# Kernel optimization log

Measured on AMD Instinct MI355X. Metric: run time of the kernel, lower is better.

The kernel has to match this reference:

```python
import jax, jax.numpy as jnp
import numpy as np

N = 10000      # nodes
E = 320000     # edges
IN_DIM = 256
HID = 256
EDGE_DIM = 64


def _sage(x, src, dst, w_l, b_l, w_r, n_nodes):
    """PyG SAGEConv (aggr='mean', root_weight=True, normalize=False):
    out_i = lin_l(mean_{j->i} x_j) + lin_r(x_i). Messages flow src->dst."""
    msg = x[src]                                            # [E, F]
    agg = jax.ops.segment_sum(msg, dst, num_segments=n_nodes)
    cnt = jax.ops.segment_sum(jnp.ones((msg.shape[0], 1), x.dtype), dst,
                              num_segments=n_nodes)
    mean = agg / jnp.maximum(cnt, 1.0)                      # [N, F]
    return mean @ w_l.T + b_l + x @ w_r.T                   # [N, HID]


def setup_inputs() -> dict:
    key = jax.random.key(0)
    ks = jax.random.split(key, 13)
    s = 0.02
    return {
        "x": jax.random.normal(ks[0], (N, IN_DIM), dtype=jnp.float32),
        "edge_attr": jax.random.normal(ks[1], (E, EDGE_DIM), dtype=jnp.float32),
        "conv1_wl": jax.random.normal(ks[2], (HID, IN_DIM), dtype=jnp.float32) * s,
        "conv1_bl": jnp.zeros((HID,), dtype=jnp.float32),
        "conv1_wr": jax.random.normal(ks[3], (HID, IN_DIM), dtype=jnp.float32) * s,
        "conv2_wl": jax.random.normal(ks[4], (HID, HID), dtype=jnp.float32) * s,
        "conv2_bl": jnp.zeros((HID,), dtype=jnp.float32),
        "conv2_wr": jax.random.normal(ks[5], (HID, HID), dtype=jnp.float32) * s,
        "mlp_w1": jax.random.normal(ks[6], (HID, 2 * HID + EDGE_DIM), dtype=jnp.float32) * s,
        "mlp_b1": jnp.zeros((HID,), dtype=jnp.float32),
        "mlp_w2": jax.random.normal(ks[7], (1, HID), dtype=jnp.float32) * s,
        "mlp_b2": jnp.zeros((1,), dtype=jnp.float32),
        "edge_index": jax.random.randint(ks[8], (2, E), 0, N, dtype=jnp.int32),
    }


def reference(x, edge_attr, conv1_wl, conv1_bl, conv1_wr,
              conv2_wl, conv2_bl, conv2_wr,
              mlp_w1, mlp_b1, mlp_w2, mlp_b2, edge_index):
    src, dst = edge_index[0], edge_index[1]
    # encode_nodes (dropout is identity in eval mode)
    h = jax.nn.relu(_sage(x, src, dst, conv1_wl, conv1_bl, conv1_wr, N))
    h = _sage(h, src, dst, conv2_wl, conv2_bl, conv2_wr, N)
    # edge_logits: gather endpoints, concat with edge_attr, 2-layer MLP
    feats = jnp.concatenate([h[src], h[dst], edge_attr], axis=1)   # [E, 2H+ED]
    hidden = jax.nn.relu(feats @ mlp_w1.T + mlp_b1)                # [E, H]
    logits = hidden @ mlp_w2.T + mlp_b2                            # [E, 1]
    return logits[:, 0]
```

## Files before the change

### kernel.cpp

```cpp
#include <hip/hip_runtime.h>

#define N_NODES 10000
#define N_EDGES 320000
#define DIM 256
#define ED 64
#define W1_LD 576

__global__ void hist_kernel(const int* __restrict__ dst, int* __restrict__ cnt, int n) {
  int i = blockIdx.x * blockDim.x + threadIdx.x;
  if (i < n) atomicAdd(&cnt[dst[i]], 1);
}

__global__ void scan_kernel(const int* __restrict__ cnt, int* __restrict__ off,
                            int* __restrict__ cursor, int n) {
  __shared__ int sm[256];
  __shared__ int carry_s;
  if (threadIdx.x == 0) carry_s = 0;
  __syncthreads();
  for (int base = 0; base < n; base += 256) {
    int i = base + threadIdx.x;
    int v = (i < n) ? cnt[i] : 0;
    sm[threadIdx.x] = v;
    __syncthreads();
    #pragma unroll
    for (int s = 1; s < 256; s <<= 1) {
      int t = (threadIdx.x >= s) ? sm[threadIdx.x - s] : 0;
      __syncthreads();
      sm[threadIdx.x] += t;
      __syncthreads();
    }
    int excl = sm[threadIdx.x] - v + carry_s;
    if (i < n) { off[i] = excl; cursor[i] = excl; }
    __syncthreads();
    if (threadIdx.x == 0) carry_s += sm[255];
    __syncthreads();
  }
  if (threadIdx.x == 0) off[n] = carry_s;
}

__global__ void scatter_kernel(const int* __restrict__ src, const int* __restrict__ dst,
                               int* __restrict__ cursor, int* __restrict__ csr_src, int n) {
  int i = blockIdx.x * blockDim.x + threadIdx.x;
  if (i < n) {
    int p = atomicAdd(&cursor[dst[i]], 1);
    csr_src[p] = src[i];
  }
}

__global__ __launch_bounds__(256) void aggregate_kernel(
    const float* __restrict__ X, const int* __restrict__ off,
    const int* __restrict__ csr_src, float* __restrict__ out) {
  int node = blockIdx.x * 4 + (threadIdx.x >> 6);
  if (node >= N_NODES) return;
  int t4 = (threadIdx.x & 63) * 4;
  int beg = off[node], end = off[node + 1];
  float ax = 0.f, ay = 0.f, az = 0.f, aw = 0.f;
  int e = beg;
  for (; e + 1 < end; e += 2) {
    int s0 = csr_src[e], s1 = csr_src[e + 1];
    float4 v0 = *(const float4*)&X[(size_t)s0 * DIM + t4];
    float4 v1 = *(const float4*)&X[(size_t)s1 * DIM + t4];
    ax += v0.x + v1.x; ay += v0.y + v1.y; az += v0.z + v1.z; aw += v0.w + v1.w;
  }
  if (e < end) {
    int s0 = csr_src[e];
    float4 v0 = *(const float4*)&X[(size_t)s0 * DIM + t4];
    ax += v0.x; ay += v0.y; az += v0.z; aw += v0.w;
  }
  int deg = end - beg;
  float inv = 1.0f / (float)(deg > 0 ? deg : 1);
  float4 r; r.x = ax * inv; r.y = ay * inv; r.z = az * inv; r.w = aw * inv;
  *(float4*)&out[(size_t)node * DIM + t4] = r;
}

template<bool SECOND, bool RELU>
__global__ __launch_bounds__(256) void gemm_kernel(
    const float* __restrict__ A1, const float* __restrict__ W1,
    const float* __restrict__ A2, const float* __restrict__ W2,
    const float* __restrict__ bias, float* __restrict__ C,
    int nrows, int K, int ldw, int ldc) {
  __shared__ float As[32][128];
  __shared__ float Bs[32][64];
  int t = threadIdx.x;
  int tx = t & 15, ty = t >> 4;
  int row0 = blockIdx.x * 128;
  int col0 = blockIdx.y * 64;

  float acc[8][4];
  #pragma unroll
  for (int i = 0; i < 8; ++i)
    #pragma unroll
    for (int j = 0; j < 4; ++j) acc[i][j] = 0.f;

  int ksteps = K / 32;
  int total = SECOND ? 2 * ksteps : ksteps;
  for (int kt = 0; kt < total; ++kt) {
    bool second = SECOND && (kt >= ksteps);
    const float* A = second ? A2 : A1;
    const float* W = second ? W2 : W1;
    int kb = (second ? (kt - ksteps) : kt) * 32;
    __syncthreads();
    #pragma unroll
    for (int i = 0; i < 4; ++i) {
      int idx = i * 256 + t;
      int m = idx >> 3;
      int kq = idx & 7;
      int row = row0 + m;
      float4 v = make_float4(0.f, 0.f, 0.f, 0.f);
      if (row < nrows) v = *(const float4*)&A[(size_t)row * K + kb + kq * 4];
      As[kq * 4 + 0][m] = v.x; As[kq * 4 + 1][m] = v.y;
      As[kq * 4 + 2][m] = v.z; As[kq * 4 + 3][m] = v.w;
    }
    #pragma unroll
    for (int i = 0; i < 2; ++i) {
      int idx = i * 256 + t;
      int o = idx >> 3;
      int kq = idx & 7;
      float4 v = *(const float4*)&W[(size_t)(col0 + o) * ldw + kb + kq * 4];
      Bs[kq * 4 + 0][o] = v.x; Bs[kq * 4 + 1][o] = v.y;
      Bs[kq * 4 + 2][o] = v.z; Bs[kq * 4 + 3][o] = v.w;
    }
    __syncthreads();
    #pragma unroll 8
    for (int k = 0; k < 32; ++k) {
      float4 a0 = *(const float4*)&As[k][ty * 4];
      float4 a1 = *(const float4*)&As[k][ty * 4 + 64];
      float4 b0 = *(const float4*)&Bs[k][tx * 4];
      float a[8] = {a0.x, a0.y, a0.z, a0.w, a1.x, a1.y, a1.z, a1.w};
      float b[4] = {b0.x, b0.y, b0.z, b0.w};
      #pragma unroll
      for (int i = 0; i < 8; ++i)
        #pragma unroll
        for (int j = 0; j < 4; ++j)
          acc[i][j] += a[i] * b[j];
    }
  }
  float4 bv = make_float4(0.f, 0.f, 0.f, 0.f);
  if (bias) bv = *(const float4*)&bias[col0 + tx * 4];
  #pragma unroll
  for (int i = 0; i < 8; ++i) {
    int m = ty * 4 + (i & 3) + (i >> 2) * 64;
    int row = row0 + m;
    if (row < nrows) {
      float4 o4;
      o4.x = acc[i][0] + bv.x; o4.y = acc[i][1] + bv.y;
      o4.z = acc[i][2] + bv.z; o4.w = acc[i][3] + bv.w;
      if (RELU) {
        o4.x = fmaxf(o4.x, 0.f); o4.y = fmaxf(o4.y, 0.f);
        o4.z = fmaxf(o4.z, 0.f); o4.w = fmaxf(o4.w, 0.f);
      }
      *(float4*)&C[(size_t)row * ldc + col0 + tx * 4] = o4;
    }
  }
}

#define EB 64
__global__ __launch_bounds__(256) void edge_kernel(
    const float* __restrict__ edge_attr,
    const int* __restrict__ src, const int* __restrict__ dst,
    const float* __restrict__ PQ,
    const float* __restrict__ mlp_w1,
    const float* __restrict__ w2,
    const float* __restrict__ b2,
    float* __restrict__ out) {
  __shared__ float w_lds[64][128];
  __shared__ float ea_lds[64][EB];
  __shared__ int sid[2][EB];
  __shared__ float w2_lds[256];

  int t = threadIdx.x;
  int e0 = blockIdx.x * EB;
  w2_lds[t] = w2[t];
  if (t < EB) { sid[0][t] = src[e0 + t]; sid[1][t] = dst[e0 + t]; }
  {
    int e_l = t >> 2, q = t & 3;
    const float* ep = &edge_attr[(size_t)(e0 + e_l) * ED + q * 16];
    #pragma unroll
    for (int j = 0; j < 4; ++j) {
      float4 v = *(const float4*)&ep[j * 4];
      int k = q * 16 + j * 4;
      ea_lds[k + 0][e_l] = v.x; ea_lds[k + 1][e_l] = v.y;
      ea_lds[k + 2][e_l] = v.z; ea_lds[k + 3][e_l] = v.w;
    }
  }
  int c = t & 15, r = t >> 4;
  float logit[4] = {0.f, 0.f, 0.f, 0.f};

  for (int half = 0; half < 2; ++half) {
    __syncthreads();
    #pragma unroll
    for (int i = 0; i < 8; ++i) {
      int idx = i * 256 + t;
      int o = idx & 127;
      int kq = idx >> 7;
      float4 v = *(const float4*)&mlp_w1[(size_t)(half * 128 + o) * W1_LD + 512 + kq * 4];
      w_lds[kq * 4 + 0][o] = v.x; w_lds[kq * 4 + 1][o] = v.y;
      w_lds[kq * 4 + 2][o] = v.z; w_lds[kq * 4 + 3][o] = v.w;
    }
    __syncthreads();
    float acc[4][8];
    #pragma unroll
    for (int i = 0; i < 4; ++i)
      #pragma unroll
      for (int j = 0; j < 8; ++j) acc[i][j] = 0.f;
    #pragma unroll 8
    for (int k = 0; k < 64; ++k) {
      float4 a = *(const float4*)&ea_lds[k][r * 4];
      float4 w0 = *(const float4*)&w_lds[k][c * 4];
      float4 w1v = *(const float4*)&w_lds[k][c * 4 + 64];
      float av[4] = {a.x, a.y, a.z, a.w};
      float wv[8] = {w0.x, w0.y, w0.z, w0.w, w1v.x, w1v.y, w1v.z, w1v.w};
      #pragma unroll
      for (int i = 0; i < 4; ++i)
        #pragma unroll
        for (int j = 0; j < 8; ++j)
          acc[i][j] += av[i] * wv[j];
    }
    float4 w2a = *(const float4*)&w2_lds[half * 128 + c * 4];
    float4 w2b = *(const float4*)&w2_lds[half * 128 + c * 4 + 64];
    float w2v[8] = {w2a.x, w2a.y, w2a.z, w2a.w, w2b.x, w2b.y, w2b.z, w2b.w};
    #pragma unroll
    for (int i = 0; i < 4; ++i) {
      int el = r * 4 + i;
      int sp = sid[0][el], dp = sid[1][el];
      const float* prow = &PQ[(size_t)sp * 512 + half * 128 + c * 4];
      const float* qrow = &PQ[(size_t)dp * 512 + 256 + half * 128 + c * 4];
      float4 p0 = *(const float4*)&prow[0];
      float4 p1 = *(const float4*)&prow[64];
      float4 q0 = *(const float4*)&qrow[0];
      float4 q1 = *(const float4*)&qrow[64];
      float pv[8] = {p0.x, p0.y, p0.z, p0.w, p1.x, p1.y, p1.z, p1.w};
      float qv[8] = {q0.x, q0.y, q0.z, q0.w, q1.x, q1.y, q1.z, q1.w};
      #pragma unroll
      for (int j = 0; j < 8; ++j) {
        float s = acc[i][j] + pv[j] + qv[j];
        s = fmaxf(s, 0.f);
        logit[i] += s * w2v[j];
      }
    }
  }
  #pragma unroll
  for (int m = 1; m < 16; m <<= 1) {
    #pragma unroll
    for (int i = 0; i < 4; ++i) logit[i] += __shfl_xor(logit[i], m, 64);
  }
  if (c == 0) {
    float bb = b2[0];
    #pragma unroll
    for (int i = 0; i < 4; ++i) out[e0 + r * 4 + i] = logit[i] + bb;
  }
}

static inline size_t alignup(size_t x) { return (x + 255) & ~(size_t)255; }

extern "C" void kernel_launch(void* const* d_in, const int* in_sizes, int n_in,
                              void* d_out, int out_size, void* d_ws, size_t ws_size,
                              hipStream_t stream) {
  const float* x    = (const float*)d_in[0];
  const float* ea   = (const float*)d_in[1];
  const float* c1wl = (const float*)d_in[2];
  const float* c1bl = (const float*)d_in[3];
  const float* c1wr = (const float*)d_in[4];
  const float* c2wl = (const float*)d_in[5];
  const float* c2bl = (const float*)d_in[6];
  const float* c2wr = (const float*)d_in[7];
  const float* w1   = (const float*)d_in[8];
  const float* b1   = (const float*)d_in[9];
  const float* w2   = (const float*)d_in[10];
  const float* b2   = (const float*)d_in[11];
  const int*   ei   = (const int*)d_in[12];
  const int* src = ei;
  const int* dst = ei + N_EDGES;
  float* out = (float*)d_out;

  char* p = (char*)d_ws;
  size_t o = 0;
  int* cnt      = (int*)(p + o); o += alignup(N_NODES * 4);
  int* off      = (int*)(p + o); o += alignup((N_NODES + 1) * 4);
  int* cursor   = (int*)(p + o); o += alignup(N_NODES * 4);
  int* csr_src  = (int*)(p + o); o += alignup(N_EDGES * 4);
  float* mbuf   = (float*)(p + o); o += alignup((size_t)N_NODES * DIM * 4);
  float* h1     = (float*)(p + o); o += alignup((size_t)N_NODES * DIM * 4);
  float* h2     = (float*)(p + o); o += alignup((size_t)N_NODES * DIM * 4);
  float* PQ     = (float*)(p + o); o += alignup((size_t)N_NODES * 512 * 4);

  hipMemsetAsync(cnt, 0, N_NODES * 4, stream);
  hist_kernel<<<(N_EDGES + 255) / 256, 256, 0, stream>>>(dst, cnt, N_EDGES);
  scan_kernel<<<1, 256, 0, stream>>>(cnt, off, cursor, N_NODES);
  scatter_kernel<<<(N_EDGES + 255) / 256, 256, 0, stream>>>(src, dst, cursor, csr_src, N_EDGES);

  dim3 ggrid((N_NODES + 127) / 128, 4);

  aggregate_kernel<<<(N_NODES + 3) / 4, 256, 0, stream>>>(x, off, csr_src, mbuf);
  gemm_kernel<true, true><<<ggrid, 256, 0, stream>>>(
      mbuf, c1wl, x, c1wr, c1bl, h1, N_NODES, DIM, DIM, DIM);

  aggregate_kernel<<<(N_NODES + 3) / 4, 256, 0, stream>>>(h1, off, csr_src, mbuf);
  gemm_kernel<true, false><<<ggrid, 256, 0, stream>>>(
      mbuf, c2wl, h1, c2wr, c2bl, h2, N_NODES, DIM, DIM, DIM);

  gemm_kernel<false, false><<<ggrid, 256, 0, stream>>>(
      h2, w1, h2, w1, b1, PQ, N_NODES, DIM, W1_LD, 512);
  gemm_kernel<false, false><<<ggrid, 256, 0, stream>>>(
      h2, w1 + 256, h2, w1 + 256, nullptr, PQ + 256, N_NODES, DIM, W1_LD, 512);

  edge_kernel<<<N_EDGES / EB, 256, 0, stream>>>(ea, src, dst, PQ, w1, w2, b2, out);
}
```

Measured before the change: 712.3 us.

## Prefetch edge gathers, merge PQ GEMMs, unroll aggregation, shuffle-based scan

The edge kernel now issues its PQ row gathers before the edge-attribute matmul and prefetches the second half during the first, reading w2 directly instead of staging it in LDS. The two PQ projection GEMMs become one launch whose upper column blocks shift the weight pointer. The aggregation loop uses four independent accumulators to raise memory-level parallelism, and the scan uses wavefront shuffles instead of LDS barriers. The extra prefetch registers may reduce occupancy in the edge kernel.

```diff
diff --git a/kernel.cpp b/kernel.cpp
--- a/kernel.cpp
+++ b/kernel.cpp
@@ -13,29 +13,32 @@
 
 __global__ void scan_kernel(const int* __restrict__ cnt, int* __restrict__ off,
                             int* __restrict__ cursor, int n) {
-  __shared__ int sm[256];
+  __shared__ int wsum[4];
   __shared__ int carry_s;
-  if (threadIdx.x == 0) carry_s = 0;
+  int t = threadIdx.x, lane = t & 63, w = t >> 6;
+  if (t == 0) carry_s = 0;
   __syncthreads();
   for (int base = 0; base < n; base += 256) {
-    int i = base + threadIdx.x;
+    int i = base + t;
     int v = (i < n) ? cnt[i] : 0;
-    sm[threadIdx.x] = v;
-    __syncthreads();
-    #pragma unroll
-    for (int s = 1; s < 256; s <<= 1) {
-      int t = (threadIdx.x >= s) ? sm[threadIdx.x - s] : 0;
-      __syncthreads();
-      sm[threadIdx.x] += t;
-      __syncthreads();
-    }
-    int excl = sm[threadIdx.x] - v + carry_s;
+    int sc = v;
+    #pragma unroll
+    for (int s = 1; s < 64; s <<= 1) {
+      int u = __shfl_up(sc, s, 64);
+      if (lane >= s) sc += u;
+    }
+    if (lane == 63) wsum[w] = sc;
+    __syncthreads();
+    int woff = 0, tot = 0;
+    #pragma unroll
+    for (int j = 0; j < 4; ++j) { int s = wsum[j]; if (j < w) woff += s; tot += s; }
+    int excl = sc - v + woff + carry_s;
     if (i < n) { off[i] = excl; cursor[i] = excl; }
     __syncthreads();
-    if (threadIdx.x == 0) carry_s += sm[255];
-    __syncthreads();
-  }
-  if (threadIdx.x == 0) off[n] = carry_s;
+    if (t == 0) carry_s += tot;
+    __syncthreads();
+  }
+  if (t == 0) off[n] = carry_s;
 }
 
 __global__ void scatter_kernel(const int* __restrict__ src, const int* __restrict__ dst,
@@ -51,40 +54,55 @@
     const float* __restrict__ X, const int* __restrict__ off,
     const int* __restrict__ csr_src, float* __restrict__ out) {
   int node = blockIdx.x * 4 + (threadIdx.x >> 6);
-  if (node >= N_NODES) return;
   int t4 = (threadIdx.x & 63) * 4;
   int beg = off[node], end = off[node + 1];
-  float ax = 0.f, ay = 0.f, az = 0.f, aw = 0.f;
+  float x0=0.f,y0=0.f,z0=0.f,w0=0.f, x1=0.f,y1=0.f,z1=0.f,w1=0.f;
+  float x2=0.f,y2=0.f,z2=0.f,w2=0.f, x3=0.f,y3=0.f,z3=0.f,w3=0.f;
   int e = beg;
-  for (; e + 1 < end; e += 2) {
-    int s0 = csr_src[e], s1 = csr_src[e + 1];
+  for (; e + 3 < end; e += 4) {
+    int s0 = csr_src[e], s1 = csr_src[e+1], s2 = csr_src[e+2], s3 = csr_src[e+3];
     float4 v0 = *(const float4*)&X[(size_t)s0 * DIM + t4];
     float4 v1 = *(const float4*)&X[(size_t)s1 * DIM + t4];
-    ax += v0.x + v1.x; ay += v0.y + v1.y; az += v0.z + v1.z; aw += v0.w + v1.w;
-  }
-  if (e < end) {
-    int s0 = csr_src[e];
-    float4 v0 = *(const float4*)&X[(size_t)s0 * DIM + t4];
-    ax += v0.x; ay += v0.y; az += v0.z; aw += v0.w;
+    float4 v2 = *(const float4*)&X[(size_t)s2 * DIM + t4];
+    float4 v3 = *(const float4*)&X[(size_t)s3 * DIM + t4];
+    x0+=v0.x; y0+=v0.y; z0+=v0.z; w0+=v0.w;
+    x1+=v1.x; y1+=v1.y; z1+=v1.z; w1+=v1.w;
+    x2+=v2.x; y2+=v2.y; z2+=v2.z; w2+=v2.w;
+    x3+=v3.x; y3+=v3.y; z3+=v3.z; w3+=v3.w;
+  }
+  for (; e < end; ++e) {
+    int s = csr_src[e];
+    float4 v = *(const float4*)&X[(size_t)s * DIM + t4];
+    x0+=v.x; y0+=v.y; z0+=v.z; w0+=v.w;
   }
   int deg = end - beg;
   float inv = 1.0f / (float)(deg > 0 ? deg : 1);
-  float4 r; r.x = ax * inv; r.y = ay * inv; r.z = az * inv; r.w = aw * inv;
+  float4 r;
+  r.x = (x0+x1+x2+x3) * inv; r.y = (y0+y1+y2+y3) * inv;
+  r.z = (z0+z1+z2+z3) * inv; r.w = (w0+w1+w2+w3) * inv;
   *(float4*)&out[(size_t)node * DIM + t4] = r;
 }
 
 template<bool SECOND, bool RELU>
 __global__ __launch_bounds__(256) void gemm_kernel(
-    const float* __restrict__ A1, const float* __restrict__ W1,
-    const float* __restrict__ A2, const float* __restrict__ W2,
+    const float* __restrict__ W1_, const float* __restrict__ A1,
+    const float* __restrict__ A2, const float* __restrict__ W2_,
     const float* __restrict__ bias, float* __restrict__ C,
-    int nrows, int K, int ldw, int ldc) {
+    int nrows, int K, int ldw, int ldc, int wsplit) {
   __shared__ float As[32][128];
   __shared__ float Bs[32][64];
   int t = threadIdx.x;
   int tx = t & 15, ty = t >> 4;
   int row0 = blockIdx.x * 128;
   int col0 = blockIdx.y * 64;
+
+  const float* W1 = W1_;
+  const float* W2 = W2_;
+  bool qreg = (col0 >= wsplit);
+  if (qreg) {
+    ptrdiff_t adj = (ptrdiff_t)wsplit - (ptrdiff_t)wsplit * (ptrdiff_t)ldw;
+    W1 = W1_ + adj; W2 = W2_ + adj;
+  }
 
   float acc[8][4];
   #pragma unroll
@@ -136,7 +154,7 @@
     }
   }
   float4 bv = make_float4(0.f, 0.f, 0.f, 0.f);
-  if (bias) bv = *(const float4*)&bias[col0 + tx * 4];
+  if (bias && !qreg) bv = *(const float4*)&bias[col0 + tx * 4];
   #pragma unroll
   for (int i = 0; i < 8; ++i) {
     int m = ty * 4 + (i & 3) + (i >> 2) * 64;
@@ -166,11 +184,9 @@
   __shared__ float w_lds[64][128];
   __shared__ float ea_lds[64][EB];
   __shared__ int sid[2][EB];
-  __shared__ float w2_lds[256];
 
   int t = threadIdx.x;
   int e0 = blockIdx.x * EB;
-  w2_lds[t] = w2[t];
   if (t < EB) { sid[0][t] = src[e0 + t]; sid[1][t] = dst[e0 + t]; }
   {
     int e_l = t >> 2, q = t & 3;
@@ -185,9 +201,27 @@
   }
   int c = t & 15, r = t >> 4;
   float logit[4] = {0.f, 0.f, 0.f, 0.f};
+  __syncthreads();
+
+  const float* pbase[4];
+  const float* qbase[4];
+  #pragma unroll
+  for (int i = 0; i < 4; ++i) {
+    int el = r * 4 + i;
+    pbase[i] = &PQ[(size_t)sid[0][el] * 512 + c * 4];
+    qbase[i] = &PQ[(size_t)sid[1][el] * 512 + 256 + c * 4];
+  }
+
+  float4 pf[4][2], qf[4][2];
+  #pragma unroll
+  for (int i = 0; i < 4; ++i) {
+    pf[i][0] = *(const float4*)&pbase[i][0];
+    pf[i][1] = *(const float4*)&pbase[i][64];
+    qf[i][0] = *(const float4*)&qbase[i][0];
+    qf[i][1] = *(const float4*)&qbase[i][64];
+  }
 
   for (int half = 0; half < 2; ++half) {
-    __syncthreads();
     #pragma unroll
     for (int i = 0; i < 8; ++i) {
       int idx = i * 256 + t;
@@ -206,37 +240,41 @@
     #pragma unroll 8
     for (int k = 0; k < 64; ++k) {
       float4 a = *(const float4*)&ea_lds[k][r * 4];
-      float4 w0 = *(const float4*)&w_lds[k][c * 4];
-      float4 w1v = *(const float4*)&w_lds[k][c * 4 + 64];
+      float4 wv0 = *(const float4*)&w_lds[k][c * 4];
+      float4 wv1 = *(const float4*)&w_lds[k][c * 4 + 64];
       float av[4] = {a.x, a.y, a.z, a.w};
-      float wv[8] = {w0.x, w0.y, w0.z, w0.w, w1v.x, w1v.y, w1v.z, w1v.w};
+      float wv[8] = {wv0.x, wv0.y, wv0.z, wv0.w, wv1.x, wv1.y, wv1.z, wv1.w};
       #pragma unroll
       for (int i = 0; i < 4; ++i)
         #pragma unroll
         for (int j = 0; j < 8; ++j)
           acc[i][j] += av[i] * wv[j];
     }
-    float4 w2a = *(const float4*)&w2_lds[half * 128 + c * 4];
-    float4 w2b = *(const float4*)&w2_lds[half * 128 + c * 4 + 64];
+    float4 w2a = *(const float4*)&w2[half * 128 + c * 4];
+    float4 w2b = *(const float4*)&w2[half * 128 + c * 4 + 64];
     float w2v[8] = {w2a.x, w2a.y, w2a.z, w2a.w, w2b.x, w2b.y, w2b.z, w2b.w};
     #pragma unroll
     for (int i = 0; i < 4; ++i) {
-      int el = r * 4 + i;
-      int sp = sid[0][el], dp = sid[1][el];
-      const float* prow = &PQ[(size_t)sp * 512 + half * 128 + c * 4];
-      const float* qrow = &PQ[(size_t)dp * 512 + 256 + half * 128 + c * 4];
-      float4 p0 = *(const float4*)&prow[0];
-      float4 p1 = *(const float4*)&prow[64];
-      float4 q0 = *(const float4*)&qrow[0];
-      float4 q1 = *(const float4*)&qrow[64];
-      float pv[8] = {p0.x, p0.y, p0.z, p0.w, p1.x, p1.y, p1.z, p1.w};
-      float qv[8] = {q0.x, q0.y, q0.z, q0.w, q1.x, q1.y, q1.z, q1.w};
+      float pv[8] = {pf[i][0].x, pf[i][0].y, pf[i][0].z, pf[i][0].w,
+                     pf[i][1].x, pf[i][1].y, pf[i][1].z, pf[i][1].w};
+      float qv[8] = {qf[i][0].x, qf[i][0].y, qf[i][0].z, qf[i][0].w,
+                     qf[i][1].x, qf[i][1].y, qf[i][1].z, qf[i][1].w};
       #pragma unroll
       for (int j = 0; j < 8; ++j) {
         float s = acc[i][j] + pv[j] + qv[j];
         s = fmaxf(s, 0.f);
         logit[i] += s * w2v[j];
       }
+    }
+    if (half == 0) {
+      #pragma unroll
+      for (int i = 0; i < 4; ++i) {
+        pf[i][0] = *(const float4*)&pbase[i][128];
+        pf[i][1] = *(const float4*)&pbase[i][192];
+        qf[i][0] = *(const float4*)&qbase[i][128];
+        qf[i][1] = *(const float4*)&qbase[i][192];
+      }
+      __syncthreads();
     }
   }
   #pragma unroll
@@ -290,19 +328,19 @@
   scatter_kernel<<<(N_EDGES + 255) / 256, 256, 0, stream>>>(src, dst, cursor, csr_src, N_EDGES);
 
   dim3 ggrid((N_NODES + 127) / 128, 4);
-
-  aggregate_kernel<<<(N_NODES + 3) / 4, 256, 0, stream>>>(x, off, csr_src, mbuf);
+  dim3 pqgrid((N_NODES + 127) / 128, 8);
+  const int NOSPLIT = 1 << 30;
+
+  aggregate_kernel<<<N_NODES / 4, 256, 0, stream>>>(x, off, csr_src, mbuf);
   gemm_kernel<true, true><<<ggrid, 256, 0, stream>>>(
-      mbuf, c1wl, x, c1wr, c1bl, h1, N_NODES, DIM, DIM, DIM);
-
-  aggregate_kernel<<<(N_NODES + 3) / 4, 256, 0, stream>>>(h1, off, csr_src, mbuf);
+      c1wl, mbuf, x, c1wr, c1bl, h1, N_NODES, DIM, DIM, DIM, NOSPLIT);
+
+  aggregate_kernel<<<N_NODES / 4, 256, 0, stream>>>(h1, off, csr_src, mbuf);
   gemm_kernel<true, false><<<ggrid, 256, 0, stream>>>(
-      mbuf, c2wl, h1, c2wr, c2bl, h2, N_NODES, DIM, DIM, DIM);
-
-  gemm_kernel<false, false><<<ggrid, 256, 0, stream>>>(
-      h2, w1, h2, w1, b1, PQ, N_NODES, DIM, W1_LD, 512);
-  gemm_kernel<false, false><<<ggrid, 256, 0, stream>>>(
-      h2, w1 + 256, h2, w1 + 256, nullptr, PQ + 256, N_NODES, DIM, W1_LD, 512);
+      c2wl, mbuf, h1, c2wr, c2bl, h2, N_NODES, DIM, DIM, DIM, NOSPLIT);
+
+  gemm_kernel<false, false><<<pqgrid, 256, 0, stream>>>(
+      w1, h2, h2, w1, b1, PQ, N_NODES, DIM, W1_LD, 512, 256);
 
   edge_kernel<<<N_EDGES / EB, 256, 0, stream>>>(ea, src, dst, PQ, w1, w2, b2, out);
 }
```

Measured after the change: 663.9 us. -6.8%, faster.
